# Optimization experiments

Measured on AMD Instinct MI355X. Metric: run time of the kernel, lower is better.

Reference implementation:

```python
import jax, jax.numpy as jnp
import numpy as np

D_MODEL = 1536
N_HEADS = 12
HEAD_DIM = D_MODEL // N_HEADS  # 128
H_GROUP = N_HEADS // 3         # 4
B, T = 2, 2048
ROPE_THETA = 1000000.0
EPS = 1.1920928955078125e-07   # torch.finfo(float32).eps (nn.RMSNorm default)


def setup_inputs() -> dict:
    key = jax.random.key(0)
    ks = jax.random.split(key, 12)
    pdim = H_GROUP * HEAD_DIM
    s_in = 1.0 / np.sqrt(D_MODEL)
    inp = {"hidden_states": jax.random.normal(ks[0], (B, T, D_MODEL), jnp.float32)}
    names = ["wq_f", "wk_f", "wv_f", "wq_b", "wk_b", "wv_b", "wq_d", "wk_d", "wv_d"]
    for i, n in enumerate(names):
        inp[n] = jax.random.normal(ks[1 + i], (pdim, D_MODEL), jnp.float32) * s_in
    inp["wo"] = jax.random.normal(ks[10], (D_MODEL, N_HEADS * HEAD_DIM), jnp.float32) * s_in
    inp["q_norm_w"] = jnp.ones((HEAD_DIM,), jnp.float32)
    inp["k_norm_w"] = jnp.ones((HEAD_DIM,), jnp.float32)
    ii = jnp.arange(T)
    inp["forward_mask"] = ii[:, None] >= ii[None, :]   # causal
    inp["backward_mask"] = ii[:, None] <= ii[None, :]  # anti-causal
    inp["bidirectional_mask"] = jnp.ones((T, T), bool)
    return inp


def _rmsnorm(x, w):
    return x * jax.lax.rsqrt(jnp.mean(x * x, axis=-1, keepdims=True) + EPS) * w


def _rotate_half(x):
    x1, x2 = jnp.split(x, 2, axis=-1)
    return jnp.concatenate([-x2, x1], axis=-1)


def _rope_tables(seq_len):
    inv_freq = 1.0 / (ROPE_THETA ** (jnp.arange(0, HEAD_DIM, 2, dtype=jnp.float32) / HEAD_DIM))
    freqs = jnp.outer(jnp.arange(seq_len, dtype=jnp.float32), inv_freq)
    emb = jnp.concatenate([freqs, freqs], axis=-1)  # [T, head_dim]
    return jnp.cos(emb), jnp.sin(emb)


def _project_rope(x, wq, wk, wv, q_norm_w, k_norm_w, cos, sin):
    Bq, Tq, _ = x.shape
    def proj(w):
        return (x @ w.T).reshape(Bq, Tq, H_GROUP, HEAD_DIM).transpose(0, 2, 1, 3)
    q, k, v = proj(wq), proj(wk), proj(wv)
    q = _rmsnorm(q, q_norm_w)
    k = _rmsnorm(k, k_norm_w)
    c = cos[None, None]  # [1,1,T,hd]
    s = sin[None, None]
    q = q * c + _rotate_half(q) * s
    k = k * c + _rotate_half(k) * s
    return q, k, v


def _attn(q, k, v, mask):
    scale = 1.0 / np.sqrt(HEAD_DIM)
    scores = jnp.einsum("bhqd,bhkd->bhqk", q, k) * scale
    scores = jnp.where(mask[None, None], scores, -jnp.inf)
    w = jax.nn.softmax(scores, axis=-1)
    return jnp.einsum("bhqk,bhkd->bhqd", w, v)


def reference(hidden_states, wq_f, wk_f, wv_f, wq_b, wk_b, wv_b, wq_d, wk_d, wv_d,
              wo, q_norm_w, k_norm_w, forward_mask, backward_mask, bidirectional_mask):
    Bq, Tq, _ = hidden_states.shape
    cos, sin = _rope_tables(Tq)
    outs = []
    for (wq, wk, wv, m) in [(wq_f, wk_f, wv_f, forward_mask),
                            (wq_b, wk_b, wv_b, backward_mask),
                            (wq_d, wk_d, wv_d, bidirectional_mask)]:
        q, k, v = _project_rope(hidden_states, wq, wk, wv, q_norm_w, k_norm_w, cos, sin)
        a = _attn(q, k, v, m)  # [B,h,T,hd]
        outs.append(a.transpose(0, 2, 1, 3).reshape(Bq, Tq, H_GROUP * HEAD_DIM))
    attn_concat = jnp.concatenate(outs, axis=-1)
    return attn_concat @ wo.T
```

## Files before the change

kernel.cpp:

```cpp
#include <hip/hip_runtime.h>
#include <stdint.h>
#include <stddef.h>

typedef __attribute__((ext_vector_type(8))) short bf16x8;
typedef __attribute__((ext_vector_type(4))) float f32x4;
typedef __attribute__((ext_vector_type(16))) float f32x16;

#define DMODEL 1536
#define TSEQ   2048
#define HDIM   128
#define NBR    3
#define NHB    4
#define MROWS  4096

__device__ __forceinline__ float bf2f(unsigned short u) {
  union { unsigned int i; float f; } v; v.i = ((unsigned int)u) << 16; return v.f;
}
__device__ __forceinline__ unsigned short f2bf(float f) {
  union { float f; unsigned int i; } v; v.f = f;
  unsigned int r = v.i + 0x7fffu + ((v.i >> 16) & 1u);
  return (unsigned short)(r >> 16);
}
__device__ __forceinline__ unsigned int cvtpk(float lo, float hi) {
  unsigned int r;
  asm("v_cvt_pk_bf16_f32 %0, %1, %2" : "=v"(r) : "v"(lo), "v"(hi));
  return r;
}
__device__ __forceinline__ void plswap(unsigned int& a, unsigned int& b) {
  asm("v_permlane32_swap_b32 %0, %1" : "+v"(a), "+v"(b));
}
__device__ __forceinline__ void gload_lds16(const void* g, void* l) {
  __builtin_amdgcn_global_load_lds((__attribute__((address_space(1))) void*)g,
                                   (__attribute__((address_space(3))) void*)l,
                                   16, 0, 0);
}

__global__ __launch_bounds__(256) void k_cvt(const float* __restrict__ src,
                                             unsigned short* __restrict__ dst,
                                             int n4) {
  int i = blockIdx.x * 256 + threadIdx.x;
  if (i >= n4) return;
  float4 v = ((const float4*)src)[i];
  ushort4 o;
  o.x = f2bf(v.x); o.y = f2bf(v.y); o.z = f2bf(v.z); o.w = f2bf(v.w);
  ((ushort4*)dst)[i] = o;
}

struct W9 { const float* w[9]; };

__global__ __launch_bounds__(256) void k_cvt9(W9 ws, unsigned short* __restrict__ dst,
                                              int n4) {
  int seg = blockIdx.y;
  const float* __restrict__ src = ws.w[seg];
  unsigned short* __restrict__ d = dst + (size_t)seg * (size_t)n4 * 4;
  int i = blockIdx.x * 256 + threadIdx.x;
  if (i >= n4) return;
  float4 v = ((const float4*)src)[i];
  ushort4 o;
  o.x = f2bf(v.x); o.y = f2bf(v.y); o.z = f2bf(v.z); o.w = f2bf(v.w);
  ((ushort4*)d)[i] = o;
}

#define GBM 128
#define GBN 192
#define GBK 64
#define GK  1536
#define GNT (GK / GBK)

template<int EPI>
__global__ __launch_bounds__(512, 4) void k_gemm8(
    const unsigned short* __restrict__ A, const unsigned short* __restrict__ Bw,
    unsigned short* __restrict__ Qs, unsigned short* __restrict__ Ksl,
    unsigned short* __restrict__ Vs, float* __restrict__ Cout)
{
  __shared__ __align__(16) unsigned short As[2 * GBM * GBK];
  __shared__ __align__(16) unsigned short Bs[2 * GBN * GBK];

  const int t = threadIdx.x, ln = t & 63, w = t >> 6;
  const int wm = w >> 2, wn = w & 3, g = ln >> 4, li = ln & 15;

  const int nwg = gridDim.x * gridDim.y;
  const int lid = blockIdx.y * gridDim.x + blockIdx.x;
  const int s = (lid & 7) * (nwg >> 3) + (lid >> 3);
  const int m0 = (s & 31) * GBM;
  const int n0 = (s >> 5) * GBN;

  f32x4 zero4 = {0.f, 0.f, 0.f, 0.f};
  f32x4 acc[4][3];
#pragma unroll
  for (int i = 0; i < 4; ++i)
#pragma unroll
    for (int j = 0; j < 3; ++j) acc[i][j] = zero4;

  auto STAGE = [&](int p, int kt) {
    const unsigned short* Ag = A + (size_t)m0 * GK + kt * GBK;
    unsigned short* Al = As + p * (GBM * GBK);
#pragma unroll
    for (int i = 0; i < 2; ++i) {
      int ch = i * 512 + t; int r = ch >> 3, c = ch & 7;
      gload_lds16(Ag + (size_t)r * GK + ((c ^ (r & 7)) * 8), Al + ch * 8);
    }
    const unsigned short* Bg = Bw + (size_t)n0 * GK + kt * GBK;
    unsigned short* Bl = Bs + p * (GBN * GBK);
#pragma unroll
    for (int i = 0; i < 3; ++i) {
      int ch = i * 512 + t; int r = ch >> 3, c = ch & 7;
      gload_lds16(Bg + (size_t)r * GK + ((c ^ (r & 7)) * 8), Bl + ch * 8);
    }
  };

  STAGE(0, 0);
  STAGE(1, 1);

  for (int kt = 0; kt < GNT; ++kt) {
    const int cur = kt & 1;
    if (kt < GNT - 1) { asm volatile("s_waitcnt vmcnt(5)" ::: "memory"); }
    else              { asm volatile("s_waitcnt vmcnt(0)" ::: "memory"); }
    __builtin_amdgcn_sched_barrier(0);
    __builtin_amdgcn_s_barrier();
    __builtin_amdgcn_sched_barrier(0);
    asm volatile("" ::: "memory");

    const unsigned short* Al = As + cur * (GBM * GBK);
    const unsigned short* Bl = Bs + cur * (GBN * GBK);
#pragma unroll
    for (int kh = 0; kh < 2; ++kh) {
      bf16x8 af[4], bfn[3];
#pragma unroll
      for (int mf = 0; mf < 4; ++mf) {
        int r = wm * 64 + mf * 16 + li;
        af[mf] = *(const bf16x8*)(Al + r * 64 + (((kh * 4 + g) ^ (li & 7)) * 8));
      }
#pragma unroll
      for (int nf = 0; nf < 3; ++nf) {
        int r = wn * 48 + nf * 16 + li;
        bfn[nf] = *(const bf16x8*)(Bl + r * 64 + (((kh * 4 + g) ^ (li & 7)) * 8));
      }
      __builtin_amdgcn_s_setprio(1);
#pragma unroll
      for (int mf = 0; mf < 4; ++mf)
#pragma unroll
        for (int nf = 0; nf < 3; ++nf)
          acc[mf][nf] = __builtin_amdgcn_mfma_f32_16x16x32_bf16(
              af[mf], bfn[nf], acc[mf][nf], 0, 0, 0);
      __builtin_amdgcn_s_setprio(0);
    }
    asm volatile("" ::: "memory");
    __builtin_amdgcn_sched_barrier(0);
    __builtin_amdgcn_s_barrier();
    __builtin_amdgcn_sched_barrier(0);
    if (kt + 2 < GNT) STAGE(cur, kt + 2);
  }

#pragma unroll
  for (int mf = 0; mf < 4; ++mf)
#pragma unroll
    for (int nf = 0; nf < 3; ++nf)
#pragma unroll
      for (int rr = 0; rr < 4; ++rr) {
        int row = m0 + wm * 64 + mf * 16 + g * 4 + rr;
        int col = n0 + wn * 48 + nf * 16 + li;
        if (EPI == 0) {
          int mat = col >> 9, within = col & 511;
          int br = mat / 3, qkv = mat % 3;
          int b = row >> 11, tt = row & 2047;
          int h = within >> 7, d = within & 127;
          unsigned short* dst = (qkv == 0) ? Qs : (qkv == 1) ? Ksl : Vs;
          size_t off = ((size_t)((br * 2 + b) * 4 + h) * TSEQ + tt) * HDIM + d;
          dst[off] = f2bf(acc[mf][nf][rr]);
        } else {
          Cout[(size_t)row * DMODEL + col] = acc[mf][nf][rr];
        }
      }
}

__global__ __launch_bounds__(256) void k_rope(
    unsigned short* __restrict__ Q, unsigned short* __restrict__ K,
    const float* __restrict__ qw, const float* __restrict__ kw)
{
  const int t = threadIdx.x, ln = t & 63, w = t >> 6;
  const int rid = blockIdx.x * 4 + w;
  const int tt  = rid & (TSEQ - 1);
  const size_t base = (size_t)rid * HDIM;

  const float ang = (float)tt * exp2f(-0.31143075464f * (float)ln);
  float s, c;
  sincosf(ang, &s, &c);

#pragma unroll
  for (int which = 0; which < 2; ++which) {
    unsigned short* P = which ? K : Q;
    const float* Wn = which ? kw : qw;
    float x1 = bf2f(P[base + ln]);
    float x2 = bf2f(P[base + 64 + ln]);
    float ss = x1 * x1 + x2 * x2;
#pragma unroll
    for (int off = 1; off < 64; off <<= 1) ss += __shfl_xor(ss, off, 64);
    float rr = rsqrtf(ss * (1.0f / 128.0f) + 1.1920928955078125e-07f);
    float y1 = x1 * rr * Wn[ln];
    float y2 = x2 * rr * Wn[64 + ln];
    P[base + ln]      = f2bf(y1 * c - y2 * s);
    P[base + 64 + ln] = f2bf(y2 * c + y1 * s);
  }
}

__global__ __launch_bounds__(256) void k_vtrans(
    const unsigned short* __restrict__ V, unsigned short* __restrict__ VT)
{
  __shared__ unsigned short L[64 * 65];
  const int tb = blockIdx.x;
  const int db = blockIdx.y;
  const int sl = blockIdx.z;
  const size_t slab = (size_t)sl * (TSEQ * HDIM);
  const int t = threadIdx.x;

#pragma unroll
  for (int i = 0; i < 2; ++i) {
    int c = i * 256 + t;
    int trow = c >> 3, d0 = (c & 7) * 8;
    bf16x8 vv = *(const bf16x8*)(V + slab + (size_t)(tb*64 + trow) * HDIM + db*64 + d0);
#pragma unroll
    for (int j = 0; j < 8; ++j) L[trow * 65 + d0 + j] = (unsigned short)vv[j];
  }
  __syncthreads();
#pragma unroll
  for (int i = 0; i < 2; ++i) {
    int c = i * 256 + t;
    int drow = c >> 3, t0 = (c & 7) * 8;
    bf16x8 ov;
#pragma unroll
    for (int j = 0; j < 8; ++j) ov[j] = (short)L[(t0 + j) * 65 + drow];
    *(bf16x8*)(VT + slab + (size_t)(db*64 + drow) * TSEQ + tb*64 + t0) = ov;
  }
}

#define ATT_SCALE 0.08838834764831845f

template<int MODE>
__device__ __forceinline__ void flash_phase(
    int qt, int bh,
    const unsigned short* __restrict__ Q, const unsigned short* __restrict__ K,
    const unsigned short* __restrict__ VT, unsigned short* __restrict__ AO,
    unsigned short* SH)
{
  const int b = bh >> 2, h = bh & 3;
  const int t = threadIdx.x, l = t & 63, w = t >> 6;
  const int hi = l >> 5, l31 = l & 31;
  const int wq = w & 3, gid = w >> 2;
  const size_t slab = (size_t)(MODE * 8 + bh) * (TSEQ * HDIM);
  const int q0 = qt * 128;

  unsigned short* KsG = SH + gid * 17920;
  unsigned short* VtG = KsG + 8704;

  bf16x8 qf[8];
  {
    const unsigned short* qp = Q + slab + (size_t)(q0 + wq*32 + l31) * HDIM + hi*8;
#pragma unroll
    for (int st = 0; st < 8; ++st) qf[st] = *(const bf16x8*)(qp + st*16);
  }

  f32x16 zero16;
#pragma unroll
  for (int e = 0; e < 16; ++e) zero16[e] = 0.f;
  f32x16 acc[4];
#pragma unroll
  for (int df = 0; df < 4; ++df) acc[df] = zero16;
  float m_run = -1e30f, l_run = 0.f;

  int n, ktbase, diagAt;
  if (MODE == 0)      { n = qt + 1;  ktbase = gid;          diagAt = n - 1; }
  else if (MODE == 1) { n = 16 - qt; ktbase = 2*qt + gid;   diagAt = 0; }
  else                { n = 16;      ktbase = gid;          diagAt = -1; }

  const int tl = t & 255;
  bf16x8 rk[4], rv[4];
  auto LOADT = [&](int kt) {
    const int k0 = kt * 64;
#pragma unroll
    for (int j = 0; j < 4; ++j) {
      int c = j * 256 + tl;
      rk[j] = *(const bf16x8*)(K  + slab + (size_t)(k0 + (c >> 4)) * HDIM + (c & 15) * 8);
      rv[j] = *(const bf16x8*)(VT + slab + (size_t)(c >> 3) * TSEQ + k0 + (c & 7) * 8);
    }
  };

  LOADT(ktbase);

  for (int i = 0; i < n; ++i) {
    const int kt = ktbase + 2 * i;
    const int k0 = kt * 64;
    __syncthreads();
#pragma unroll
    for (int j = 0; j < 4; ++j) {
      int c = j * 256 + tl;
      *(bf16x8*)(KsG + (c >> 4) * 136 + (c & 15) * 8) = rk[j];
      *(bf16x8*)(VtG + (c >> 3) * 72  + (c & 7) * 8)  = rv[j];
    }
    if (i + 1 < n) LOADT(kt + 2);
    __syncthreads();

    f32x16 sf0 = zero16, sf1 = zero16;
#pragma unroll
    for (int st = 0; st < 8; ++st) {
      bf16x8 kf0 = *(const bf16x8*)(KsG + l31 * 136 + st*16 + hi*8);
      bf16x8 kf1 = *(const bf16x8*)(KsG + (32 + l31) * 136 + st*16 + hi*8);
      __builtin_amdgcn_s_setprio(1);
      sf0 = __builtin_amdgcn_mfma_f32_32x32x16_bf16(kf0, qf[st], sf0, 0, 0, 0);
      sf1 = __builtin_amdgcn_mfma_f32_32x32x16_bf16(kf1, qf[st], sf1, 0, 0, 0);
      __builtin_amdgcn_s_setprio(0);
    }

    float pf[32];
#pragma unroll
    for (int r = 0; r < 16; ++r) { pf[r] = sf0[r] * ATT_SCALE; pf[16+r] = sf1[r] * ATT_SCALE; }

    if (MODE != 2 && i == diagAt) {
      const int qg = q0 + wq*32 + l31;
#pragma unroll
      for (int f = 0; f < 2; ++f)
#pragma unroll
        for (int r = 0; r < 16; ++r) {
          int kg = k0 + f*32 + 4*hi + (r & 3) + 8*(r >> 2);
          bool ok = (MODE == 0) ? (kg <= qg) : (kg >= qg);
          if (!ok) pf[f*16 + r] = -1e30f;
        }
    }

    float m = pf[0];
#pragma unroll
    for (int j = 1; j < 32; ++j) m = fmaxf(m, pf[j]);
    m = fmaxf(m, __shfl_xor(m, 32, 64));

    if (__any(m > m_run)) {
      float mn = fmaxf(m_run, m);
      float alpha = __expf(m_run - mn);
      m_run = mn;
      l_run *= alpha;
#pragma unroll
      for (int df = 0; df < 4; ++df) acc[df] *= alpha;
    }

    float rs0 = 0.f, rs1 = 0.f, rs2 = 0.f, rs3 = 0.f;
#pragma unroll
    for (int j = 0; j < 8; ++j) { pf[j]      = __expf(pf[j]      - m_run); rs0 += pf[j]; }
#pragma unroll
    for (int j = 8; j < 16; ++j){ pf[j]      = __expf(pf[j]      - m_run); rs1 += pf[j]; }
#pragma unroll
    for (int j = 0; j < 8; ++j) { pf[16+j]   = __expf(pf[16+j]   - m_run); rs2 += pf[16+j]; }
#pragma unroll
    for (int j = 8; j < 16; ++j){ pf[16+j]   = __expf(pf[16+j]   - m_run); rs3 += pf[16+j]; }
    float rs = (rs0 + rs1) + (rs2 + rs3);
    rs += __shfl_xor(rs, 32, 64);
    l_run += rs;

    unsigned int pb[2][8];
#pragma unroll
    for (int f = 0; f < 2; ++f) {
#pragma unroll
      for (int u = 0; u < 4; ++u) {
        pb[f][2*u]   = cvtpk(pf[f*16 + 4*u + 0], pf[f*16 + 4*u + 1]);
        pb[f][2*u+1] = cvtpk(pf[f*16 + 4*u + 2], pf[f*16 + 4*u + 3]);
      }
      plswap(pb[f][0], pb[f][2]);
      plswap(pb[f][1], pb[f][3]);
      plswap(pb[f][4], pb[f][6]);
      plswap(pb[f][5], pb[f][7]);
    }

#pragma unroll
    for (int s = 0; s < 4; ++s) {
      union { unsigned int u[4]; bf16x8 v; } pbv;
#pragma unroll
      for (int u = 0; u < 4; ++u) pbv.u[u] = pb[s >> 1][(s & 1) * 4 + u];
#pragma unroll
      for (int df = 0; df < 4; ++df) {
        bf16x8 vb = *(const bf16x8*)(VtG + (df*32 + l31) * 72 + s*16 + hi*8);
        __builtin_amdgcn_s_setprio(1);
        acc[df] = __builtin_amdgcn_mfma_f32_32x32x16_bf16(vb, pbv.v, acc[df], 0, 0, 0);
        __builtin_amdgcn_s_setprio(0);
      }
    }
  }

  __syncthreads();
  float* EXf = (float*)SH;
  float* MLf = (float*)(SH + 35840);
  if (gid == 1) {
    MLf[(wq*64 + l)*2 + 0] = m_run;
    MLf[(wq*64 + l)*2 + 1] = l_run;
#pragma unroll
    for (int df = 0; df < 4; ++df)
#pragma unroll
      for (int u = 0; u < 4; ++u) {
        f32x4 ch = {acc[df][4*u], acc[df][4*u+1], acc[df][4*u+2], acc[df][4*u+3]};
        *(f32x4*)&EXf[(wq*64 + l)*68 + df*16 + u*4] = ch;
      }
  }
  __syncthreads();
  if (gid == 0) {
    float mB = MLf[(wq*64 + l)*2 + 0];
    float lB = MLf[(wq*64 + l)*2 + 1];
    float mF = fmaxf(m_run, mB);
    float a0 = __expf(m_run - mF), a1 = __expf(mB - mF);
    float inv = 1.0f / (l_run * a0 + lB * a1);
    a0 *= inv; a1 *= inv;
#pragma unroll
    for (int df = 0; df < 4; ++df)
#pragma unroll
      for (int u = 0; u < 4; ++u) {
        f32x4 cb = *(const f32x4*)&EXf[(wq*64 + l)*68 + df*16 + u*4];
#pragma unroll
        for (int e = 0; e < 4; ++e)
          acc[df][4*u+e] = acc[df][4*u+e] * a0 + cb[e] * a1;
      }
  }
  __syncthreads();

  unsigned int* OT = (unsigned int*)SH;
  if (gid == 0) {
#pragma unroll
    for (int df = 0; df < 4; ++df)
#pragma unroll
      for (int u = 0; u < 4; ++u) {
        unsigned int d0 = cvtpk(acc[df][4*u+0], acc[df][4*u+1]);
        unsigned int d1 = cvtpk(acc[df][4*u+2], acc[df][4*u+3]);
        uint2 dd; dd.x = d0; dd.y = d1;
        *(uint2*)&OT[(wq*32 + l31)*68 + df*16 + 2*hi + 4*u] = dd;
      }
  }
  __syncthreads();
  {
    const int q = t >> 2, sg = t & 3;
    size_t rowbase = ((size_t)b * TSEQ + q0 + q) * DMODEL + MODE * 512 + h * HDIM;
#pragma unroll
    for (int u = 0; u < 4; ++u) {
      bf16x8 vv = *(const bf16x8*)&OT[q*68 + u*16 + sg*4];
      *(bf16x8*)(AO + rowbase + (u*16 + sg*4)*2) = vv;
    }
  }
}

__global__ __launch_bounds__(512, 2) void k_attn(
    const unsigned short* __restrict__ Q, const unsigned short* __restrict__ K,
    const unsigned short* __restrict__ VT, unsigned short* __restrict__ AO)
{
  __shared__ __align__(16) unsigned short SH[36864];

  const int qt = blockIdx.x;
  const int bh = blockIdx.y;
  if (blockIdx.z == 0) {
    flash_phase<0>(qt, bh, Q, K, VT, AO, SH);
    flash_phase<1>(qt, bh, Q, K, VT, AO, SH);
  } else {
    flash_phase<2>(qt, bh, Q, K, VT, AO, SH);
  }
}

extern "C" void kernel_launch(void* const* d_in, const int* in_sizes, int n_in,
                              void* d_out, int out_size, void* d_ws, size_t ws_size,
                              hipStream_t stream)
{
  (void)in_sizes; (void)n_in; (void)out_size; (void)ws_size;
  const float* Xf  = (const float*)d_in[0];
  const float* WOf = (const float*)d_in[10];
  const float* qw  = (const float*)d_in[11];
  const float* kw  = (const float*)d_in[12];

  const size_t S = (size_t)NBR * 2 * NHB * TSEQ * HDIM;
  unsigned short* Qs   = (unsigned short*)d_ws;
  unsigned short* Ks   = Qs + S;
  unsigned short* Vs   = Ks + S;
  unsigned short* AO   = Vs + S;
  unsigned short* Xbf  = AO + S;
  unsigned short* Wbf  = Xbf + (size_t)MROWS * DMODEL;
  unsigned short* WObf = Wbf + (size_t)9 * 512 * DMODEL;
  unsigned short* VTs  = Xbf;
  float* Cout = (float*)d_out;

  dim3 blk(256);

  k_cvt<<<dim3((MROWS * DMODEL) / 1024), blk, 0, stream>>>(Xf, Xbf, (MROWS * DMODEL) / 4);
  W9 w9;
  for (int i = 0; i < 9; ++i) w9.w[i] = (const float*)d_in[1 + i];
  k_cvt9<<<dim3((512 * DMODEL) / 1024, 9), blk, 0, stream>>>(w9, Wbf, (512 * DMODEL) / 4);
  k_cvt<<<dim3((DMODEL * DMODEL) / 1024), blk, 0, stream>>>(WOf, WObf, (DMODEL * DMODEL) / 4);

  k_gemm8<0><<<dim3(32, 24), dim3(512), 0, stream>>>(Xbf, Wbf, Qs, Ks, Vs, nullptr);
  k_rope<<<dim3(12288), blk, 0, stream>>>(Qs, Ks, qw, kw);
  k_vtrans<<<dim3(32, 2, 24), blk, 0, stream>>>(Vs, VTs);
  k_attn<<<dim3(16, 8, 2), dim3(512), 0, stream>>>(Qs, Ks, VTs, AO);
  k_gemm8<1><<<dim3(32, 8), dim3(512), 0, stream>>>(AO, WObf, nullptr, nullptr, nullptr, Cout);
}
```

Before: 191.6 us.

## Fuse V transpose into QKV GEMM epilogue and load B operand directly to registers

The QKV projection GEMM now writes V straight into the transposed [d][t] layout with 4-wide packed stores, so the separate V-transpose kernel and its launch are removed. The B (weight) tile no longer goes through LDS; each wave loads its B fragments from global memory into double-buffered registers, and the K loop is unrolled by two to alternate between them. This cuts LDS traffic and shared-memory footprint, but raises register pressure and makes B reads non-coalesced global loads that are duplicated across waves.

After: 421.0 us. 120% more time.

```diff
diff --git a/kernel.cpp b/kernel.cpp
--- a/kernel.cpp
+++ b/kernel.cpp
@@ -74,7 +74,6 @@
     unsigned short* __restrict__ Vs, float* __restrict__ Cout)
 {
   __shared__ __align__(16) unsigned short As[2 * GBM * GBK];
-  __shared__ __align__(16) unsigned short Bs[2 * GBN * GBK];
 
   const int t = threadIdx.x, ln = t & 63, w = t >> 6;
   const int wm = w >> 2, wn = w & 3, g = ln >> 4, li = ln & 15;
@@ -92,7 +91,7 @@
 #pragma unroll
     for (int j = 0; j < 3; ++j) acc[i][j] = zero4;
 
-  auto STAGE = [&](int p, int kt) {
+  auto ASTAGE = [&](int p, int kt) {
     const unsigned short* Ag = A + (size_t)m0 * GK + kt * GBK;
     unsigned short* Al = As + p * (GBM * GBK);
 #pragma unroll
@@ -100,78 +99,86 @@
       int ch = i * 512 + t; int r = ch >> 3, c = ch & 7;
       gload_lds16(Ag + (size_t)r * GK + ((c ^ (r & 7)) * 8), Al + ch * 8);
     }
-    const unsigned short* Bg = Bw + (size_t)n0 * GK + kt * GBK;
-    unsigned short* Bl = Bs + p * (GBN * GBK);
-#pragma unroll
-    for (int i = 0; i < 3; ++i) {
-      int ch = i * 512 + t; int r = ch >> 3, c = ch & 7;
-      gload_lds16(Bg + (size_t)r * GK + ((c ^ (r & 7)) * 8), Bl + ch * 8);
-    }
   };
-
-  STAGE(0, 0);
-  STAGE(1, 1);
-
-  for (int kt = 0; kt < GNT; ++kt) {
+  auto BLOAD = [&](int kt, bf16x8 (&BB)[3][2]) {
+    const unsigned short* Bg = Bw + (size_t)n0 * GK + (size_t)kt * GBK;
+#pragma unroll
+    for (int nf = 0; nf < 3; ++nf)
+#pragma unroll
+      for (int kh = 0; kh < 2; ++kh)
+        BB[nf][kh] = *(const bf16x8*)(Bg + (size_t)(wn*48 + nf*16 + li) * GK + (kh*4 + g) * 8);
+  };
+
+  auto GBODY = [&](int kt, bf16x8 (&BB)[3][2]) {
     const int cur = kt & 1;
-    if (kt < GNT - 1) { asm volatile("s_waitcnt vmcnt(5)" ::: "memory"); }
+    if (kt < GNT - 1) { asm volatile("s_waitcnt vmcnt(8)" ::: "memory"); }
     else              { asm volatile("s_waitcnt vmcnt(0)" ::: "memory"); }
     __builtin_amdgcn_sched_barrier(0);
     __builtin_amdgcn_s_barrier();
     __builtin_amdgcn_sched_barrier(0);
-    asm volatile("" ::: "memory");
 
     const unsigned short* Al = As + cur * (GBM * GBK);
-    const unsigned short* Bl = Bs + cur * (GBN * GBK);
 #pragma unroll
     for (int kh = 0; kh < 2; ++kh) {
-      bf16x8 af[4], bfn[3];
+      bf16x8 af[4];
 #pragma unroll
       for (int mf = 0; mf < 4; ++mf) {
         int r = wm * 64 + mf * 16 + li;
         af[mf] = *(const bf16x8*)(Al + r * 64 + (((kh * 4 + g) ^ (li & 7)) * 8));
       }
-#pragma unroll
-      for (int nf = 0; nf < 3; ++nf) {
-        int r = wn * 48 + nf * 16 + li;
-        bfn[nf] = *(const bf16x8*)(Bl + r * 64 + (((kh * 4 + g) ^ (li & 7)) * 8));
-      }
       __builtin_amdgcn_s_setprio(1);
 #pragma unroll
       for (int mf = 0; mf < 4; ++mf)
 #pragma unroll
         for (int nf = 0; nf < 3; ++nf)
           acc[mf][nf] = __builtin_amdgcn_mfma_f32_16x16x32_bf16(
-              af[mf], bfn[nf], acc[mf][nf], 0, 0, 0);
+              af[mf], BB[nf][kh], acc[mf][nf], 0, 0, 0);
       __builtin_amdgcn_s_setprio(0);
     }
-    asm volatile("" ::: "memory");
     __builtin_amdgcn_sched_barrier(0);
     __builtin_amdgcn_s_barrier();
     __builtin_amdgcn_sched_barrier(0);
-    if (kt + 2 < GNT) STAGE(cur, kt + 2);
+    if (kt + 2 < GNT) { ASTAGE(cur, kt + 2); BLOAD(kt + 2, BB); }
+  };
+
+  bf16x8 B0[3][2], B1[3][2];
+  ASTAGE(0, 0); BLOAD(0, B0);
+  ASTAGE(1, 1); BLOAD(1, B1);
+
+  for (int kt2 = 0; kt2 < GNT; kt2 += 2) {
+    GBODY(kt2, B0);
+    GBODY(kt2 + 1, B1);
   }
 
 #pragma unroll
   for (int mf = 0; mf < 4; ++mf)
 #pragma unroll
-    for (int nf = 0; nf < 3; ++nf)
-#pragma unroll
-      for (int rr = 0; rr < 4; ++rr) {
-        int row = m0 + wm * 64 + mf * 16 + g * 4 + rr;
-        int col = n0 + wn * 48 + nf * 16 + li;
-        if (EPI == 0) {
-          int mat = col >> 9, within = col & 511;
-          int br = mat / 3, qkv = mat % 3;
-          int b = row >> 11, tt = row & 2047;
-          int h = within >> 7, d = within & 127;
-          unsigned short* dst = (qkv == 0) ? Qs : (qkv == 1) ? Ksl : Vs;
-          size_t off = ((size_t)((br * 2 + b) * 4 + h) * TSEQ + tt) * HDIM + d;
-          dst[off] = f2bf(acc[mf][nf][rr]);
+    for (int nf = 0; nf < 3; ++nf) {
+      int row0 = m0 + wm * 64 + mf * 16 + g * 4;
+      int col  = n0 + wn * 48 + nf * 16 + li;
+      if (EPI == 0) {
+        int mat = col >> 9, within = col & 511;
+        int br = mat / 3, qkv = mat % 3;
+        int h = within >> 7, d = within & 127;
+        int b = row0 >> 11, tt0 = row0 & 2047;
+        size_t slabI = (size_t)((br * 2 + b) * 4 + h) * (TSEQ * HDIM);
+        if (qkv == 2) {
+          ushort4 o;
+          o.x = f2bf(acc[mf][nf][0]); o.y = f2bf(acc[mf][nf][1]);
+          o.z = f2bf(acc[mf][nf][2]); o.w = f2bf(acc[mf][nf][3]);
+          *(ushort4*)(Vs + slabI + (size_t)d * TSEQ + tt0) = o;
         } else {
-          Cout[(size_t)row * DMODEL + col] = acc[mf][nf][rr];
+          unsigned short* dst = (qkv == 0) ? Qs : Ksl;
+#pragma unroll
+          for (int rr = 0; rr < 4; ++rr)
+            dst[slabI + (size_t)(tt0 + rr) * HDIM + d] = f2bf(acc[mf][nf][rr]);
         }
-      }
+      } else {
+#pragma unroll
+        for (int rr = 0; rr < 4; ++rr)
+          Cout[(size_t)(row0 + rr) * DMODEL + col] = acc[mf][nf][rr];
+      }
+    }
 }
 
 __global__ __launch_bounds__(256) void k_rope(
@@ -201,36 +208,6 @@
     float y2 = x2 * rr * Wn[64 + ln];
     P[base + ln]      = f2bf(y1 * c - y2 * s);
     P[base + 64 + ln] = f2bf(y2 * c + y1 * s);
-  }
-}
-
-__global__ __launch_bounds__(256) void k_vtrans(
-    const unsigned short* __restrict__ V, unsigned short* __restrict__ VT)
-{
-  __shared__ unsigned short L[64 * 65];
-  const int tb = blockIdx.x;
-  const int db = blockIdx.y;
-  const int sl = blockIdx.z;
-  const size_t slab = (size_t)sl * (TSEQ * HDIM);
-  const int t = threadIdx.x;
-
-#pragma unroll
-  for (int i = 0; i < 2; ++i) {
-    int c = i * 256 + t;
-    int trow = c >> 3, d0 = (c & 7) * 8;
-    bf16x8 vv = *(const bf16x8*)(V + slab + (size_t)(tb*64 + trow) * HDIM + db*64 + d0);
-#pragma unroll
-    for (int j = 0; j < 8; ++j) L[trow * 65 + d0 + j] = (unsigned short)vv[j];
-  }
-  __syncthreads();
-#pragma unroll
-  for (int i = 0; i < 2; ++i) {
-    int c = i * 256 + t;
-    int drow = c >> 3, t0 = (c & 7) * 8;
-    bf16x8 ov;
-#pragma unroll
-    for (int j = 0; j < 8; ++j) ov[j] = (short)L[(t0 + j) * 65 + drow];
-    *(bf16x8*)(VT + slab + (size_t)(db*64 + drow) * TSEQ + tb*64 + t0) = ov;
   }
 }
 
@@ -343,13 +320,13 @@
 
     float rs0 = 0.f, rs1 = 0.f, rs2 = 0.f, rs3 = 0.f;
 #pragma unroll
-    for (int j = 0; j < 8; ++j) { pf[j]      = __expf(pf[j]      - m_run); rs0 += pf[j]; }
-#pragma unroll
-    for (int j = 8; j < 16; ++j){ pf[j]      = __expf(pf[j]      - m_run); rs1 += pf[j]; }
-#pragma unroll
-    for (int j = 0; j < 8; ++j) { pf[16+j]   = __expf(pf[16+j]   - m_run); rs2 += pf[16+j]; }
-#pragma unroll
-    for (int j = 8; j < 16; ++j){ pf[16+j]   = __expf(pf[16+j]   - m_run); rs3 += pf[16+j]; }
+    for (int j = 0; j < 8; ++j) { pf[j]    = __expf(pf[j]    - m_run); rs0 += pf[j]; }
+#pragma unroll
+    for (int j = 8; j < 16; ++j){ pf[j]    = __expf(pf[j]    - m_run); rs1 += pf[j]; }
+#pragma unroll
+    for (int j = 0; j < 8; ++j) { pf[16+j] = __expf(pf[16+j] - m_run); rs2 += pf[16+j]; }
+#pragma unroll
+    for (int j = 8; j < 16; ++j){ pf[16+j] = __expf(pf[16+j] - m_run); rs3 += pf[16+j]; }
     float rs = (rs0 + rs1) + (rs2 + rs3);
     rs += __shfl_xor(rs, 32, 64);
     l_run += rs;
@@ -475,7 +452,6 @@
   unsigned short* Xbf  = AO + S;
   unsigned short* Wbf  = Xbf + (size_t)MROWS * DMODEL;
   unsigned short* WObf = Wbf + (size_t)9 * 512 * DMODEL;
-  unsigned short* VTs  = Xbf;
   float* Cout = (float*)d_out;
 
   dim3 blk(256);
@@ -488,7 +464,6 @@
 
   k_gemm8<0><<<dim3(32, 24), dim3(512), 0, stream>>>(Xbf, Wbf, Qs, Ks, Vs, nullptr);
   k_rope<<<dim3(12288), blk, 0, stream>>>(Qs, Ks, qw, kw);
-  k_vtrans<<<dim3(32, 2, 24), blk, 0, stream>>>(Vs, VTs);
-  k_attn<<<dim3(16, 8, 2), dim3(512), 0, stream>>>(Qs, Ks, VTs, AO);
+  k_attn<<<dim3(16, 8, 2), dim3(512), 0, stream>>>(Qs, Ks, Vs, AO);
   k_gemm8<1><<<dim3(32, 8), dim3(512), 0, stream>>>(AO, WObf, nullptr, nullptr, nullptr, Cout);
 }
```

## Load GEMM B operand directly from global into registers, bypassing LDS

Applied to the files above, without the earlier changes.

The projection GEMM no longer stages the weight (B) tile through shared memory. Each wave loads its own B fragments straight from global memory into double-buffered registers, two k-steps ahead, and the k-loop is unrolled by two so the buffers alternate. This removes the B traffic through LDS and the LDS reads, and shrinks shared memory use. The cost is more registers, more uncoalesced global loads, and duplicate B loads across the waves that share a column block (wm=0/1), which may pressure occupancy under launch bounds of 512 threads with 4 blocks.

After: 426.3 us, median of 2. +122.5%, slower.

```diff
diff --git a/kernel.cpp b/kernel.cpp
--- a/kernel.cpp
+++ b/kernel.cpp
@@ -74,7 +74,6 @@
     unsigned short* __restrict__ Vs, float* __restrict__ Cout)
 {
   __shared__ __align__(16) unsigned short As[2 * GBM * GBK];
-  __shared__ __align__(16) unsigned short Bs[2 * GBN * GBK];
 
   const int t = threadIdx.x, ln = t & 63, w = t >> 6;
   const int wm = w >> 2, wn = w & 3, g = ln >> 4, li = ln & 15;
@@ -92,7 +91,7 @@
 #pragma unroll
     for (int j = 0; j < 3; ++j) acc[i][j] = zero4;
 
-  auto STAGE = [&](int p, int kt) {
+  auto ASTAGE = [&](int p, int kt) {
     const unsigned short* Ag = A + (size_t)m0 * GK + kt * GBK;
     unsigned short* Al = As + p * (GBM * GBK);
 #pragma unroll
@@ -100,56 +99,55 @@
       int ch = i * 512 + t; int r = ch >> 3, c = ch & 7;
       gload_lds16(Ag + (size_t)r * GK + ((c ^ (r & 7)) * 8), Al + ch * 8);
     }
-    const unsigned short* Bg = Bw + (size_t)n0 * GK + kt * GBK;
-    unsigned short* Bl = Bs + p * (GBN * GBK);
-#pragma unroll
-    for (int i = 0; i < 3; ++i) {
-      int ch = i * 512 + t; int r = ch >> 3, c = ch & 7;
-      gload_lds16(Bg + (size_t)r * GK + ((c ^ (r & 7)) * 8), Bl + ch * 8);
-    }
   };
-
-  STAGE(0, 0);
-  STAGE(1, 1);
-
-  for (int kt = 0; kt < GNT; ++kt) {
+  auto BLOAD = [&](int kt, bf16x8 (&BB)[3][2]) {
+    const unsigned short* Bg = Bw + (size_t)n0 * GK + (size_t)kt * GBK;
+#pragma unroll
+    for (int nf = 0; nf < 3; ++nf)
+#pragma unroll
+      for (int kh = 0; kh < 2; ++kh)
+        BB[nf][kh] = *(const bf16x8*)(Bg + (size_t)(wn*48 + nf*16 + li) * GK + (kh*4 + g) * 8);
+  };
+
+  auto GBODY = [&](int kt, bf16x8 (&BB)[3][2]) {
     const int cur = kt & 1;
-    if (kt < GNT - 1) { asm volatile("s_waitcnt vmcnt(5)" ::: "memory"); }
+    if (kt < GNT - 1) { asm volatile("s_waitcnt vmcnt(8)" ::: "memory"); }
     else              { asm volatile("s_waitcnt vmcnt(0)" ::: "memory"); }
     __builtin_amdgcn_sched_barrier(0);
     __builtin_amdgcn_s_barrier();
     __builtin_amdgcn_sched_barrier(0);
-    asm volatile("" ::: "memory");
 
     const unsigned short* Al = As + cur * (GBM * GBK);
-    const unsigned short* Bl = Bs + cur * (GBN * GBK);
 #pragma unroll
     for (int kh = 0; kh < 2; ++kh) {
-      bf16x8 af[4], bfn[3];
+      bf16x8 af[4];
 #pragma unroll
       for (int mf = 0; mf < 4; ++mf) {
         int r = wm * 64 + mf * 16 + li;
         af[mf] = *(const bf16x8*)(Al + r * 64 + (((kh * 4 + g) ^ (li & 7)) * 8));
       }
-#pragma unroll
-      for (int nf = 0; nf < 3; ++nf) {
-        int r = wn * 48 + nf * 16 + li;
-        bfn[nf] = *(const bf16x8*)(Bl + r * 64 + (((kh * 4 + g) ^ (li & 7)) * 8));
-      }
       __builtin_amdgcn_s_setprio(1);
 #pragma unroll
       for (int mf = 0; mf < 4; ++mf)
 #pragma unroll
         for (int nf = 0; nf < 3; ++nf)
           acc[mf][nf] = __builtin_amdgcn_mfma_f32_16x16x32_bf16(
-              af[mf], bfn[nf], acc[mf][nf], 0, 0, 0);
+              af[mf], BB[nf][kh], acc[mf][nf], 0, 0, 0);
       __builtin_amdgcn_s_setprio(0);
     }
-    asm volatile("" ::: "memory");
     __builtin_amdgcn_sched_barrier(0);
     __builtin_amdgcn_s_barrier();
     __builtin_amdgcn_sched_barrier(0);
-    if (kt + 2 < GNT) STAGE(cur, kt + 2);
+    if (kt + 2 < GNT) { ASTAGE(cur, kt + 2); BLOAD(kt + 2, BB); }
+  };
+
+  bf16x8 B0[3][2], B1[3][2];
+  ASTAGE(0, 0); BLOAD(0, B0);
+  ASTAGE(1, 1); BLOAD(1, B1);
+
+  for (int kt2 = 0; kt2 < GNT; kt2 += 2) {
+    GBODY(kt2, B0);
+    GBODY(kt2 + 1, B1);
   }
 
 #pragma unroll
@@ -343,13 +341,13 @@
 
     float rs0 = 0.f, rs1 = 0.f, rs2 = 0.f, rs3 = 0.f;
 #pragma unroll
-    for (int j = 0; j < 8; ++j) { pf[j]      = __expf(pf[j]      - m_run); rs0 += pf[j]; }
-#pragma unroll
-    for (int j = 8; j < 16; ++j){ pf[j]      = __expf(pf[j]      - m_run); rs1 += pf[j]; }
-#pragma unroll
-    for (int j = 0; j < 8; ++j) { pf[16+j]   = __expf(pf[16+j]   - m_run); rs2 += pf[16+j]; }
-#pragma unroll
-    for (int j = 8; j < 16; ++j){ pf[16+j]   = __expf(pf[16+j]   - m_run); rs3 += pf[16+j]; }
+    for (int j = 0; j < 8; ++j) { pf[j]    = __expf(pf[j]    - m_run); rs0 += pf[j]; }
+#pragma unroll
+    for (int j = 8; j < 16; ++j){ pf[j]    = __expf(pf[j]    - m_run); rs1 += pf[j]; }
+#pragma unroll
+    for (int j = 0; j < 8; ++j) { pf[16+j] = __expf(pf[16+j] - m_run); rs2 += pf[16+j]; }
+#pragma unroll
+    for (int j = 8; j < 16; ++j){ pf[16+j] = __expf(pf[16+j] - m_run); rs3 += pf[16+j]; }
     float rs = (rs0 + rs1) + (rs2 + rs3);
     rs += __shfl_xor(rs, 32, 64);
     l_run += rs;
```
